# Optimization experiments

Hardware: AMD Instinct MI355X
Metric: run time of the kernel (lower is better)

## Reference

```python
import jax, jax.numpy as jnp
import numpy as np

B, T, D = 4, 2048, 1024
H, HS = 16, 64  # num heads, head size; H*HS == D


def setup_inputs() -> dict:
    key = jax.random.key(0)
    ks = jax.random.split(key, 6)
    scale = D ** -0.5
    x = jax.random.normal(ks[0], (B, T, D), dtype=jnp.float32)
    # per-head projections, stacked: [H, D, HS]
    Wq = jax.random.normal(ks[1], (H, D, HS), dtype=jnp.float32) * scale
    Wk = jax.random.normal(ks[2], (H, D, HS), dtype=jnp.float32) * scale
    Wv = jax.random.normal(ks[3], (H, D, HS), dtype=jnp.float32) * scale
    # output projection: [H*HS, D] + bias [D]
    Wp = jax.random.normal(ks[4], (H * HS, D), dtype=jnp.float32) * ((H * HS) ** -0.5)
    bp = jax.random.normal(ks[5], (D,), dtype=jnp.float32) * 0.01
    return {"x": x, "Wq": Wq, "Wk": Wk, "Wv": Wv, "Wp": Wp, "bp": bp}


def reference(x, Wq, Wk, Wv, Wp, bp):
    # per-head Q, K, V projections (batched over heads): [B, H, T, HS]
    q = jnp.einsum('btd,hde->bhte', x, Wq)
    k = jnp.einsum('btd,hde->bhte', x, Wk)
    v = jnp.einsum('btd,hde->bhte', x, Wv)
    # scaled scores with causal mask: [B, H, T, T]
    scores = jnp.einsum('bhte,bhse->bhts', q, k) * (HS ** -0.5)
    causal = jnp.tril(jnp.ones((T, T), dtype=bool))
    scores = jnp.where(causal, scores, jnp.float32(-jnp.inf))
    wei = jax.nn.softmax(scores, axis=-1)  # dropout is identity at eval
    out = jnp.einsum('bhts,bhse->bhte', wei, v)
    # concat heads -> [B, T, H*HS], then output projection
    out = out.transpose(0, 2, 1, 3).reshape(B, T, H * HS)
    return out @ Wp + bp
```

## Files before the change

### kernel.cpp

```cpp
#include <hip/hip_runtime.h>
#include <stdint.h>

typedef __attribute__((ext_vector_type(8))) short short8;
typedef __attribute__((ext_vector_type(4))) float f32x4;
typedef __attribute__((ext_vector_type(16))) float f32x16;

__device__ __forceinline__ unsigned short f2bf(float f) {
  unsigned u = __float_as_uint(f);
  u = u + 0x7FFFu + ((u >> 16) & 1u);
  return (unsigned short)(u >> 16);
}
__device__ __forceinline__ unsigned cvtpk_bf16(float lo, float hi) {
  unsigned r;
  asm("v_cvt_pk_bf16_f32 %0, %1, %2" : "=v"(r) : "v"(lo), "v"(hi));
  return r;
}
__device__ __forceinline__ float fast_exp2(float x) {
#if __has_builtin(__builtin_amdgcn_exp2f)
  return __builtin_amdgcn_exp2f(x);
#else
  return exp2f(x);
#endif
}
__device__ __forceinline__ void gl2lds16(const void* g, void* l) {
  __builtin_amdgcn_global_load_lds(
      (const __attribute__((address_space(1))) void*)(uintptr_t)g,
      (__attribute__((address_space(3))) void*)(uintptr_t)l, 16, 0, 0);
}

__global__ __launch_bounds__(256) void pack_all_kernel(const float* __restrict__ x,
                                                       const float* __restrict__ Wq,
                                                       const float* __restrict__ Wk,
                                                       const float* __restrict__ Wv,
                                                       const float* __restrict__ Wp,
                                                       ushort* __restrict__ xb,
                                                       ushort* __restrict__ WqkvT,
                                                       ushort* __restrict__ WpT) {
  __shared__ float tile[64][65];
  const int bid0 = blockIdx.x;
  const int tid = threadIdx.x;
  if (bid0 < 4096) {
    int i = (bid0 * 256 + tid) * 8;
    float4 a = *(const float4*)(x + i);
    float4 b = *(const float4*)(x + i + 4);
    uint4 o;
    o.x = (unsigned)f2bf(a.x) | ((unsigned)f2bf(a.y) << 16);
    o.y = (unsigned)f2bf(a.z) | ((unsigned)f2bf(a.w) << 16);
    o.z = (unsigned)f2bf(b.x) | ((unsigned)f2bf(b.y) << 16);
    o.w = (unsigned)f2bf(b.z) | ((unsigned)f2bf(b.w) << 16);
    *(uint4*)(xb + i) = o;
    return;
  }
  const int bid = bid0 - 4096;
  const int lr = tid >> 6;
  const int lc = tid & 63;
  if (bid < 768) {
    const int s = bid >> 8;
    const int rem = bid & 255;
    const int h = rem >> 4;
    const int dt = rem & 15;
    const float* W = (s == 0) ? Wq : (s == 1) ? Wk : Wv;
    const float scale = (s == 0) ? 0.18033688011f : 1.0f;
#pragma unroll
    for (int p = 0; p < 16; ++p) {
      int r = p * 4 + lr;
      tile[r][lc] = W[(size_t)(h * 1024 + dt * 64 + r) * 64 + lc];
    }
    __syncthreads();
#pragma unroll
    for (int p = 0; p < 16; ++p) {
      int e = p * 4 + lr;
      float v = tile[lc][e] * scale;
      WqkvT[(size_t)(s * 1024 + h * 64 + e) * 1024 + dt * 64 + lc] = f2bf(v);
    }
  } else {
    const int t = bid - 768;
    const int rt = t >> 4, ct = t & 15;
#pragma unroll
    for (int p = 0; p < 16; ++p) {
      int r = p * 4 + lr;
      tile[r][lc] = Wp[(size_t)(rt * 64 + r) * 1024 + ct * 64 + lc];
    }
    __syncthreads();
#pragma unroll
    for (int p = 0; p < 16; ++p) {
      int c = p * 4 + lr;
      float v = tile[lc][c];
      WpT[(size_t)(ct * 64 + c) * 1024 + rt * 64 + lc] = f2bf(v);
    }
  }
}

template <int OUT_MODE>
__global__ __launch_bounds__(256) void gemm_bt(const ushort* __restrict__ A,
                                               const ushort* __restrict__ BT,
                                               ushort* __restrict__ Cb,
                                               float* __restrict__ Cf,
                                               const float* __restrict__ bias,
                                               int M, int N, int K) {
  __shared__ __align__(16) ushort Al[128 * 64];
  __shared__ __align__(16) ushort Bl[128 * 64];
  const int tid = threadIdx.x;
  const int lane = tid & 63;
  const int wave = tid >> 6;
  const int wm = wave >> 1, wn = wave & 1;
  const int nbx = gridDim.x;
  const int nwg = nbx * gridDim.y;
  int wg = blockIdx.y * nbx + blockIdx.x;
  wg = (wg & 7) * (nwg >> 3) + (wg >> 3);
  const int m0 = (wg / nbx) * 128, n0 = (wg % nbx) * 128;
  const int r16 = lane & 15, g = lane >> 4;
  f32x4 acc[4][4] = {};
  const int kTiles = K >> 6;
  const size_t ldb = (size_t)K * 2;
  const int srow = tid >> 3;
  const int scol = ((tid & 7) * 16) ^ (((tid >> 3) & 7) << 4);
  const char* a_src = (const char*)A + (size_t)(m0 + srow) * ldb + scol;
  const char* b_src = (const char*)BT + (size_t)(n0 + srow) * ldb + scol;
  char* a_d = (char*)Al + wave * 1024;
  char* b_d = (char*)Bl + wave * 1024;
  const size_t row32 = (size_t)32 * ldb;
  for (int kt = 0; kt < kTiles; ++kt) {
    const size_t k0b = (size_t)kt * 128;
    if (kt) __syncthreads();
#pragma unroll
    for (int i = 0; i < 4; ++i) {
      gl2lds16(a_src + i * row32 + k0b, a_d + i * 4096);
      gl2lds16(b_src + i * row32 + k0b, b_d + i * 4096);
    }
    __syncthreads();
    short8 af[4][2], bf2[4][2];
#pragma unroll
    for (int i = 0; i < 4; ++i) {
      const int ra = (wm * 64 + i * 16 + r16) * 128;
      const int rb = (wn * 64 + i * 16 + r16) * 128;
      const int sw = (r16 & 7) << 4;
#pragma unroll
      for (int ks = 0; ks < 2; ++ks) {
        af[i][ks] = *(const short8*)((const char*)Al + ra + ((ks * 64 + g * 16) ^ sw));
        bf2[i][ks] = *(const short8*)((const char*)Bl + rb + ((ks * 64 + g * 16) ^ sw));
      }
    }
#pragma unroll
    for (int ks = 0; ks < 2; ++ks)
#pragma unroll
      for (int mi = 0; mi < 4; ++mi)
#pragma unroll
        for (int ni = 0; ni < 4; ++ni)
          acc[mi][ni] = __builtin_amdgcn_mfma_f32_16x16x32_bf16(af[mi][ks], bf2[ni][ks],
                                                                acc[mi][ni], 0, 0, 0);
  }
#pragma unroll
  for (int mi = 0; mi < 4; ++mi)
#pragma unroll
    for (int ni = 0; ni < 4; ++ni)
#pragma unroll
      for (int r = 0; r < 4; ++r) {
        int row = m0 + wm * 64 + mi * 16 + g * 4 + r;
        int col = n0 + wn * 64 + ni * 16 + r16;
        float v = acc[mi][ni][r];
        if (OUT_MODE == 0) {
          Cb[(size_t)row * N + col] = f2bf(v);
        } else {
          Cf[(size_t)row * N + col] = v + bias[col];
        }
      }
}

__global__ __launch_bounds__(128) void attn_mfma_kernel(const ushort* __restrict__ QKV,
                                                        ushort* __restrict__ O) {
  int flat = blockIdx.z * 256 + blockIdx.y * 16 + blockIdx.x;
  flat = (flat & 7) * 128 + (flat >> 3);
  const int qtA = flat & 15;
  const int h = (flat >> 4) & 15;
  const int b = flat >> 8;
  __shared__ __align__(16) ushort Kl[64 * 64];
  __shared__ __align__(16) ushort VT[64 * 64];
  const int tid = threadIdx.x;
  const int lane = tid & 63;
  const int wave = tid >> 6;
  const int lo5 = lane & 31;
  const int hi = lane >> 5;

  short8 ones;
#pragma unroll
  for (int i = 0; i < 8; ++i) ones[i] = (short)0x3F80;

  const int krow_off = wave * 8 + (lane >> 3);
  const int ksrc_col = ((lane & 7) * 16) ^ (((lane >> 3) & 7) << 4);
  const char* kgbase = (const char*)(QKV + ((size_t)b * 2048) * 3072 + 1024 + h * 64);
  const int kp2 = (tid & 31) * 2;
  const int dg0 = tid >> 5;
  const char* vgbase = (const char*)(QKV + ((size_t)b * 2048) * 3072 + 2048 + h * 64);

#pragma unroll
  for (int ph = 0; ph < 2; ++ph) {
    const int qt = ph ? qtA : (31 - qtA);
    const int qbase = qt * 64 + wave * 32;
    const int qg = qbase + lo5;

    short8 qf[4];
    {
      const ushort* qp = QKV + ((size_t)(b * 2048 + qbase + lo5) * 3072) + h * 64 + hi * 8;
#pragma unroll
      for (int dc = 0; dc < 4; ++dc) qf[dc] = *(const short8*)(qp + dc * 16);
    }

    f32x16 o0 = {}, o1 = {}, lacc = {};
    const int nblk = qt + 1;

    uint4 va0, va1, vb0, vb1;
    {
      const char* vp = vgbase + (size_t)kp2 * 6144 + dg0 * 16;
      va0 = *(const uint4*)vp;
      va1 = *(const uint4*)(vp + 6144);
      vb0 = *(const uint4*)(vp + 64);
      vb1 = *(const uint4*)(vp + 6144 + 64);
    }

    for (int blk = 0; blk < nblk; ++blk) {
      const int s0 = blk * 64;
      __syncthreads();
      {
        const ushort* ea0 = (const ushort*)&va0;
        const ushort* ea1 = (const ushort*)&va1;
        const ushort* eb0 = (const ushort*)&vb0;
        const ushort* eb1 = (const ushort*)&vb1;
#pragma unroll
        for (int j = 0; j < 8; ++j) {
          const int col = (kp2 * 2) ^ (j << 4);
          *(unsigned*)((char*)VT + (dg0 * 8 + j) * 128 + col) =
              (unsigned)ea0[j] | ((unsigned)ea1[j] << 16);
          *(unsigned*)((char*)VT + ((dg0 + 4) * 8 + j) * 128 + col) =
              (unsigned)eb0[j] | ((unsigned)eb1[j] << 16);
        }
      }
#pragma unroll
      for (int i = 0; i < 4; ++i) {
        gl2lds16(kgbase + (size_t)(s0 + i * 16 + krow_off) * 6144 + ksrc_col,
                 (char*)Kl + i * 2048 + wave * 1024);
      }
      __syncthreads();

      if (blk + 1 < nblk) {
        const char* vp = vgbase + (size_t)(s0 + 64 + kp2) * 6144 + dg0 * 16;
        va0 = *(const uint4*)vp;
        va1 = *(const uint4*)(vp + 6144);
        vb0 = *(const uint4*)(vp + 64);
        vb1 = *(const uint4*)(vp + 6144 + 64);
      }

#pragma unroll
      for (int g2 = 0; g2 < 2; ++g2) {
        const int ks = s0 + g2 * 32;
        if (ks > qbase + 31) continue;
        f32x16 s_acc = {};
        const int krow = g2 * 32 + lo5;
        const char* ksrc = (const char*)Kl + krow * 128;
        const int ksw = (krow & 7) << 4;
#pragma unroll
        for (int dc = 0; dc < 4; ++dc) {
          short8 kf = *(const short8*)(ksrc + ((dc * 32 + hi * 16) ^ ksw));
          s_acc = __builtin_amdgcn_mfma_f32_32x32x16_bf16(kf, qf[dc], s_acc, 0, 0, 0);
        }
        float p[16];
        if (ks + 31 > qbase) {
          const int ksg = ks + 4 * hi;
#pragma unroll
          for (int r = 0; r < 16; ++r) {
            const int key_g = ksg + (r & 3) + 8 * (r >> 2);
            float pv = fast_exp2(s_acc[r]);
            p[r] = (key_g <= qg) ? pv : 0.f;
          }
        } else {
#pragma unroll
          for (int r = 0; r < 16; ++r) p[r] = fast_exp2(s_acc[r]);
        }
#pragma unroll
        for (int kc = 0; kc < 2; ++kc) {
          unsigned w0 = cvtpk_bf16(p[kc * 8 + 0], p[kc * 8 + 1]);
          unsigned w2 = cvtpk_bf16(p[kc * 8 + 4], p[kc * 8 + 5]);
          unsigned w1 = cvtpk_bf16(p[kc * 8 + 2], p[kc * 8 + 3]);
          unsigned w3 = cvtpk_bf16(p[kc * 8 + 6], p[kc * 8 + 7]);
          asm("v_permlane32_swap_b32 %0, %1" : "+v"(w0), "+v"(w2));
          asm("v_permlane32_swap_b32 %0, %1" : "+v"(w1), "+v"(w3));
          uint4 paw;
          paw.x = w0; paw.y = w1; paw.z = w2; paw.w = w3;
          short8 pa = *(short8*)&paw;
          const int kb = (g2 * 32 + kc * 16 + hi * 8) * 2;
          lacc = __builtin_amdgcn_mfma_f32_32x32x16_bf16(pa, ones, lacc, 0, 0, 0);
          {
            const int vrow = lo5;
            short8 vf =
                *(const short8*)((const char*)VT + vrow * 128 + (kb ^ ((vrow & 7) << 4)));
            o0 = __builtin_amdgcn_mfma_f32_32x32x16_bf16(pa, vf, o0, 0, 0, 0);
          }
          {
            const int vrow = 32 + lo5;
            short8 vf =
                *(const short8*)((const char*)VT + vrow * 128 + (kb ^ ((vrow & 7) << 4)));
            o1 = __builtin_amdgcn_mfma_f32_32x32x16_bf16(pa, vf, o1, 0, 0, 0);
          }
        }
      }
    }

#pragma unroll
    for (int r = 0; r < 16; ++r) {
      const int qr = (r & 3) + 8 * (r >> 2) + 4 * hi;
      const float li = 1.f / lacc[r];
      ushort* ob = O + ((size_t)(b * 2048 + qbase + qr) * 1024) + h * 64 + lo5;
      ob[0] = f2bf(o0[r] * li);
      ob[32] = f2bf(o1[r] * li);
    }
  }
}

extern "C" void kernel_launch(void* const* d_in, const int* in_sizes, int n_in,
                              void* d_out, int out_size, void* d_ws, size_t ws_size,
                              hipStream_t stream) {
  const float* x = (const float*)d_in[0];
  const float* Wq = (const float*)d_in[1];
  const float* Wk = (const float*)d_in[2];
  const float* Wv = (const float*)d_in[3];
  const float* Wp = (const float*)d_in[4];
  const float* bp = (const float*)d_in[5];
  float* out = (float*)d_out;

  ushort* xb = (ushort*)d_ws;
  ushort* WqkvT = xb + 8388608;
  ushort* WpT = WqkvT + 3145728;
  ushort* QKV = WpT + 1048576;
  ushort* O = QKV + 25165824;

  pack_all_kernel<<<5120, 256, 0, stream>>>(x, Wq, Wk, Wv, Wp, xb, WqkvT, WpT);
  gemm_bt<0><<<dim3(24, 64), 256, 0, stream>>>(xb, WqkvT, QKV, nullptr, nullptr,
                                               8192, 3072, 1024);
  attn_mfma_kernel<<<dim3(16, 16, 4), 128, 0, stream>>>(QKV, O);
  gemm_bt<1><<<dim3(8, 64), 256, 0, stream>>>(O, WpT, nullptr, out, bp,
                                              8192, 1024, 1024);
}
```

Measured before the change: 164.8 us.

## Double-buffer K tiles in attention and widen blocks to 128 query rows

The attention kernel now uses 256 threads per block, with four waves covering 128 query rows, and half as many blocks. Each 64-key K tile is shared by twice as many waves, which halves K/V global traffic per query. K is prefetched into a second LDS buffer via global-to-LDS loads while the current tile is being computed. The trade-offs are more LDS per block and fewer blocks for load balancing on the causal triangle. Each wave now also handles a finer slice of the V transpose.

```diff
diff --git a/kernel.cpp b/kernel.cpp
--- a/kernel.cpp
+++ b/kernel.cpp
@@ -167,14 +167,14 @@
       }
 }
 
-__global__ __launch_bounds__(128) void attn_mfma_kernel(const ushort* __restrict__ QKV,
+__global__ __launch_bounds__(256) void attn_mfma_kernel(const ushort* __restrict__ QKV,
                                                         ushort* __restrict__ O) {
-  int flat = blockIdx.z * 256 + blockIdx.y * 16 + blockIdx.x;
-  flat = (flat & 7) * 128 + (flat >> 3);
-  const int qtA = flat & 15;
-  const int h = (flat >> 4) & 15;
-  const int b = flat >> 8;
-  __shared__ __align__(16) ushort Kl[64 * 64];
+  int flat = blockIdx.z * 128 + blockIdx.y * 8 + blockIdx.x;
+  flat = (flat & 7) * 64 + (flat >> 3);
+  const int qtA = flat & 7;
+  const int h = (flat >> 3) & 15;
+  const int b = flat >> 7;
+  __shared__ __align__(16) ushort Kl[2][64 * 64];
   __shared__ __align__(16) ushort VT[64 * 64];
   const int tid = threadIdx.x;
   const int lane = tid & 63;
@@ -186,17 +186,19 @@
 #pragma unroll
   for (int i = 0; i < 8; ++i) ones[i] = (short)0x3F80;
 
-  const int krow_off = wave * 8 + (lane >> 3);
-  const int ksrc_col = ((lane & 7) * 16) ^ (((lane >> 3) & 7) << 4);
+  const int k_key0 = wave * 16 + (lane >> 3);
+  const int k_key1 = k_key0 + 8;
+  const int ksrc_off0 = ((lane & 7) * 16) ^ ((k_key0 & 7) << 4);
+  const int ksrc_off1 = ((lane & 7) * 16) ^ ((k_key1 & 7) << 4);
   const char* kgbase = (const char*)(QKV + ((size_t)b * 2048) * 3072 + 1024 + h * 64);
   const int kp2 = (tid & 31) * 2;
-  const int dg0 = tid >> 5;
-  const char* vgbase = (const char*)(QKV + ((size_t)b * 2048) * 3072 + 2048 + h * 64);
+  const int dg = tid >> 5;
+  const char* vgbase = (const char*)(QKV + ((size_t)b * 2048) * 3072 + 2048 + h * 64 + dg * 8);
 
 #pragma unroll
   for (int ph = 0; ph < 2; ++ph) {
-    const int qt = ph ? qtA : (31 - qtA);
-    const int qbase = qt * 64 + wave * 32;
+    const int qt = ph ? qtA : (15 - qtA);
+    const int qbase = qt * 128 + wave * 32;
     const int qg = qbase + lo5;
 
     short8 qf[4];
@@ -207,56 +209,51 @@
     }
 
     f32x16 o0 = {}, o1 = {}, lacc = {};
-    const int nblk = qt + 1;
-
-    uint4 va0, va1, vb0, vb1;
+    const int nblk = qt * 2 + 2;
+
+    uint4 nv0, nv1;
     {
-      const char* vp = vgbase + (size_t)kp2 * 6144 + dg0 * 16;
-      va0 = *(const uint4*)vp;
-      va1 = *(const uint4*)(vp + 6144);
-      vb0 = *(const uint4*)(vp + 64);
-      vb1 = *(const uint4*)(vp + 6144 + 64);
-    }
-
+      const char* vp = vgbase + (size_t)kp2 * 6144;
+      nv0 = *(const uint4*)(vp);
+      nv1 = *(const uint4*)(vp + 6144);
+    }
+    __syncthreads();
+    gl2lds16(kgbase + (size_t)k_key0 * 6144 + ksrc_off0, (char*)Kl[0] + wave * 2048);
+    gl2lds16(kgbase + (size_t)k_key1 * 6144 + ksrc_off1, (char*)Kl[0] + wave * 2048 + 1024);
+
+    int cur = 0;
     for (int blk = 0; blk < nblk; ++blk) {
       const int s0 = blk * 64;
       __syncthreads();
       {
-        const ushort* ea0 = (const ushort*)&va0;
-        const ushort* ea1 = (const ushort*)&va1;
-        const ushort* eb0 = (const ushort*)&vb0;
-        const ushort* eb1 = (const ushort*)&vb1;
+        const ushort* e0 = (const ushort*)&nv0;
+        const ushort* e1 = (const ushort*)&nv1;
 #pragma unroll
         for (int j = 0; j < 8; ++j) {
-          const int col = (kp2 * 2) ^ (j << 4);
-          *(unsigned*)((char*)VT + (dg0 * 8 + j) * 128 + col) =
-              (unsigned)ea0[j] | ((unsigned)ea1[j] << 16);
-          *(unsigned*)((char*)VT + ((dg0 + 4) * 8 + j) * 128 + col) =
-              (unsigned)eb0[j] | ((unsigned)eb1[j] << 16);
-        }
-      }
-#pragma unroll
-      for (int i = 0; i < 4; ++i) {
-        gl2lds16(kgbase + (size_t)(s0 + i * 16 + krow_off) * 6144 + ksrc_col,
-                 (char*)Kl + i * 2048 + wave * 1024);
+          const int row = dg * 8 + j;
+          *(unsigned*)((char*)VT + row * 128 + ((kp2 * 2) ^ ((row & 7) << 4))) =
+              (unsigned)e0[j] | ((unsigned)e1[j] << 16);
+        }
       }
       __syncthreads();
 
       if (blk + 1 < nblk) {
-        const char* vp = vgbase + (size_t)(s0 + 64 + kp2) * 6144 + dg0 * 16;
-        va0 = *(const uint4*)vp;
-        va1 = *(const uint4*)(vp + 6144);
-        vb0 = *(const uint4*)(vp + 64);
-        vb1 = *(const uint4*)(vp + 6144 + 64);
-      }
-
+        char* kd = (char*)Kl[cur ^ 1] + wave * 2048;
+        gl2lds16(kgbase + (size_t)(s0 + 64 + k_key0) * 6144 + ksrc_off0, kd);
+        gl2lds16(kgbase + (size_t)(s0 + 64 + k_key1) * 6144 + ksrc_off1, kd + 1024);
+        const char* vp = vgbase + (size_t)(s0 + 64 + kp2) * 6144;
+        nv0 = *(const uint4*)(vp);
+        nv1 = *(const uint4*)(vp + 6144);
+      }
+
+      const ushort* Kb = Kl[cur];
 #pragma unroll
       for (int g2 = 0; g2 < 2; ++g2) {
         const int ks = s0 + g2 * 32;
         if (ks > qbase + 31) continue;
         f32x16 s_acc = {};
         const int krow = g2 * 32 + lo5;
-        const char* ksrc = (const char*)Kl + krow * 128;
+        const char* ksrc = (const char*)Kb + krow * 128;
         const int ksw = (krow & 7) << 4;
 #pragma unroll
         for (int dc = 0; dc < 4; ++dc) {
@@ -303,6 +300,7 @@
           }
         }
       }
+      cur ^= 1;
     }
 
 #pragma unroll
@@ -336,7 +334,7 @@
   pack_all_kernel<<<5120, 256, 0, stream>>>(x, Wq, Wk, Wv, Wp, xb, WqkvT, WpT);
   gemm_bt<0><<<dim3(24, 64), 256, 0, stream>>>(xb, WqkvT, QKV, nullptr, nullptr,
                                                8192, 3072, 1024);
-  attn_mfma_kernel<<<dim3(16, 16, 4), 128, 0, stream>>>(QKV, O);
+  attn_mfma_kernel<<<dim3(8, 16, 4), 256, 0, stream>>>(QKV, O);
   gemm_bt<1><<<dim3(8, 64), 256, 0, stream>>>(O, WpT, nullptr, out, bp,
                                               8192, 1024, 1024);
 }
```

Result: faster. 154.6 us (median of 2 runs) (-6.2%).
